# Kernel optimization log

Measured on AMD Instinct MI355X. Metric: run time of the kernel, lower is better.

Reference implementation:

```python
import jax, jax.numpy as jnp
import numpy as np

B, T, C = 4, 2048, 1024
H, HS = 16, 64  # n_heads, head_size; H*HS == C


def setup_inputs() -> dict:
    key = jax.random.key(0)
    ks = jax.random.split(key, 6)
    s = 0.02
    x = jax.random.normal(ks[0], (B, T, C), dtype=jnp.float32)
    Wq = jax.random.normal(ks[1], (H, C, HS), dtype=jnp.float32) * s
    Wk = jax.random.normal(ks[2], (H, C, HS), dtype=jnp.float32) * s
    Wv = jax.random.normal(ks[3], (H, C, HS), dtype=jnp.float32) * s
    Wo = jax.random.normal(ks[4], (C, C), dtype=jnp.float32) * s
    bo = jnp.zeros((C,), dtype=jnp.float32)
    return {"x": x, "Wq": Wq, "Wk": Wk, "Wv": Wv, "Wo": Wo, "bo": bo}


def reference(x, Wq, Wk, Wv, Wo, bo):
    # batched multi-head causal attention (math identical to per-head loop)
    q = jnp.einsum('btc,hcd->bhtd', x, Wq)  # [B,H,T,HS]
    k = jnp.einsum('btc,hcd->bhtd', x, Wk)
    v = jnp.einsum('btc,hcd->bhtd', x, Wv)
    scale = 1.0 / jnp.sqrt(jnp.asarray(HS, x.dtype))
    scores = jnp.einsum('bhtd,bhsd->bhts', q, k) * scale  # [B,H,T,T]
    causal = jnp.tril(jnp.ones((T, T), dtype=bool))
    scores = jnp.where(causal, scores, jnp.asarray(-jnp.inf, scores.dtype))
    attn = jax.nn.softmax(scores, axis=-1)
    out = jnp.einsum('bhts,bhsd->bhtd', attn, v)  # [B,H,T,HS]
    # concat heads along feature dim (head order == module list order)
    out = out.transpose(0, 2, 1, 3).reshape(B, T, C)
    return out @ Wo.T + bo
```

## Files before the change

### kernel.cpp

```cpp
#include <hip/hip_runtime.h>

typedef __attribute__((ext_vector_type(8))) short v8s;
typedef __attribute__((ext_vector_type(4))) short v4s;
typedef __attribute__((ext_vector_type(4))) float v4f;

static __device__ __forceinline__ short f2bf(float f) {
  union { float f; unsigned u; } c; c.f = f;
  unsigned r = c.u + 0x7fffu + ((c.u >> 16) & 1u);
  return (short)(r >> 16);
}

static __device__ __forceinline__ unsigned pk_bf16(float a, float b) {
  union { float f; unsigned u; } ca, cb; ca.f = a; cb.f = b;
  return ((ca.u + 0x8000u) >> 16) | ((cb.u + 0x8000u) & 0xffff0000u);
}

#if __has_builtin(__builtin_amdgcn_exp2f)
#define EXP2(x) __builtin_amdgcn_exp2f(x)
#else
#define EXP2(x) exp2f(x)
#endif

#define GLDS(gp, lp) __builtin_amdgcn_global_load_lds( \
    (const __attribute__((address_space(1))) void*)(gp), \
    (__attribute__((address_space(3))) void*)(lp), 16, 0, 0)


__global__ __launch_bounds__(256) void cast_f32_bf16(const float* __restrict__ src,
                                                     short* __restrict__ dst) {
  int idx = (blockIdx.x * 256 + threadIdx.x) * 4;
  float4 v = *(const float4*)(src + idx);
  v4s o; o.x = f2bf(v.x); o.y = f2bf(v.y); o.z = f2bf(v.z); o.w = f2bf(v.w);
  *(v4s*)(dst + idx) = o;
}

__global__ __launch_bounds__(256) void build_wt(const float* __restrict__ Wq,
                                                const float* __restrict__ Wk,
                                                const float* __restrict__ Wv,
                                                short* __restrict__ Wt) {
  __shared__ float tile[64][65];
  int blk = blockIdx.x;
  int sel = blk >> 8, rest = blk & 255;
  int h = rest >> 4, kt = rest & 15;
  const float* W = (sel == 0) ? Wq : ((sel == 1) ? Wk : Wv);
  int k0 = kt * 64;
  int tid = threadIdx.x;
  for (int i = 0; i < 4; ++i) {
    int c = i * 256 + tid;
    int row = c >> 4, c4 = (c & 15) * 4;
    float4 v = *(const float4*)(W + (size_t)h * 65536 + (size_t)(k0 + row) * 64 + c4);
    tile[row][c4 + 0] = v.x; tile[row][c4 + 1] = v.y;
    tile[row][c4 + 2] = v.z; tile[row][c4 + 3] = v.w;
  }
  __syncthreads();
  for (int i = 0; i < 2; ++i) {
    int c = i * 256 + tid;
    int d = c >> 3, k8 = (c & 7) * 8;
    v8s o;
    for (int j = 0; j < 8; ++j) o[j] = f2bf(tile[k8 + j][d]);
    *(v8s*)(Wt + (size_t)(sel * 1024 + h * 64 + d) * 1024 + k0 + k8) = o;
  }
}

__global__ __launch_bounds__(256) void transpose_v(const short* __restrict__ V,
                                                   short* __restrict__ Vt) {
  __shared__ short tile[64][72];
  int bh = blockIdx.x >> 5, tt = blockIdx.x & 31;
  int t0 = tt * 64;
  int tid = threadIdx.x;
  for (int i = 0; i < 2; ++i) {
    int c = i * 256 + tid;
    int row = c >> 3, col8 = (c & 7) * 8;
    v8s v = *(const v8s*)(V + ((size_t)(bh * 2048 + t0 + row)) * 64 + col8);
    *(v8s*)&tile[row][col8] = v;
  }
  __syncthreads();
  for (int i = 0; i < 2; ++i) {
    int c = i * 256 + tid;
    int d = c >> 3, t8 = (c & 7) * 8;
    v8s o;
    for (int j = 0; j < 8; ++j) o[j] = tile[t8 + j][d];
    *(v8s*)(Vt + ((size_t)(bh * 64 + d)) * 2048 + t0 + t8) = o;
  }
}


__global__ __launch_bounds__(256) void gemm_qkv(const short* __restrict__ Xb,
                                                const short* __restrict__ Wt,
                                                short* __restrict__ Qo,
                                                short* __restrict__ Ko,
                                                short* __restrict__ Vo) {
  __shared__ short lA[128 * 32];
  __shared__ short lB[128 * 32];
  const int tid = threadIdx.x;
  const int lane = tid & 63, quad = lane >> 4, l16 = lane & 15;
  const int wave = tid >> 6;
  const int m0 = blockIdx.x * 128, n0 = blockIdx.y * 128;
  const int wm = (wave >> 1) * 64, wn = (wave & 1) * 64;
  v4f acc[4][4];
  for (int i = 0; i < 4; ++i)
    for (int j = 0; j < 4; ++j) acc[i][j] = (v4f){0.f, 0.f, 0.f, 0.f};

  for (int k0 = 0; k0 < 1024; k0 += 32) {
    __syncthreads();
    for (int i = 0; i < 2; ++i) {
      int c = i * 256 + tid;
      int row = c >> 2, kc = c & 3;
      GLDS(Xb + (size_t)(m0 + row) * 1024 + k0 + kc * 8, lA + c * 8);
      GLDS(Wt + (size_t)(n0 + row) * 1024 + k0 + kc * 8, lB + c * 8);
    }
    __syncthreads();
    v8s a[4], b[4];
    for (int mt = 0; mt < 4; ++mt) a[mt] = *(const v8s*)&lA[(wm + mt * 16 + l16) * 32 + quad * 8];
    for (int nt = 0; nt < 4; ++nt) b[nt] = *(const v8s*)&lB[(wn + nt * 16 + l16) * 32 + quad * 8];
    for (int mt = 0; mt < 4; ++mt)
      for (int nt = 0; nt < 4; ++nt)
        acc[mt][nt] = __builtin_amdgcn_mfma_f32_16x16x32_bf16(a[mt], b[nt], acc[mt][nt], 0, 0, 0);
  }

  int selu = n0 >> 10;
  short* obase = (selu == 0) ? Qo : ((selu == 1) ? Ko : Vo);
  for (int nt = 0; nt < 4; ++nt) {
    int n = n0 + wn + nt * 16 + l16;
    int hd = n & 1023;
    int h = hd >> 6, d = hd & 63;
    for (int mt = 0; mt < 4; ++mt)
      for (int r = 0; r < 4; ++r) {
        int m = m0 + wm + mt * 16 + quad * 4 + r;
        int b_ = m >> 11, t = m & 2047;
        obase[(size_t)((b_ * 16 + h) * 2048 + t) * 64 + d] = f2bf(acc[mt][nt][r]);
      }
  }
}


__global__ __launch_bounds__(256, 2) void attn(const short* __restrict__ Q,
                                               const short* __restrict__ K,
                                               const short* __restrict__ Vt,
                                               short* __restrict__ AO) {
  __shared__ short lK[64 * 64];
  __shared__ short lV[64 * 64];
  __shared__ short lP[4 * 32 * 72];
  const int tid = threadIdx.x;
  const int w = tid >> 6, lane = tid & 63, quad = lane >> 4, l16 = lane & 15;
  const int bh = blockIdx.x & 63, pr = blockIdx.x >> 6;
  const float kexp = 0.18033688011112042f;
  const unsigned psel = 0x07060302u;
  short* pw = lP + w * (32 * 72);
  const size_t qkbase = (size_t)bh * 2048 * 64;
  const size_t vtbase = (size_t)bh * 64 * 2048;
  const int b_ = bh >> 4, h = bh & 15;

  const int r0 = tid >> 3, cp = tid & 7;
  const int cl0 = cp ^ (r0 & 7);
  const int r1 = r0 + 32;
  const int cl1 = cp ^ (r1 & 7);

  const int swz = l16 & 7;
  const int ph0 = (quad ^ swz) * 8;
  const int ph1 = ((quad + 4) ^ swz) * 8;

  for (int phase = 0; phase < 2; ++phase) {
    const int c = phase ? (15 - pr) : pr;
    const int qc = c * 128 + w * 32;

    v8s bQ[2][2];
#pragma unroll
    for (int qs = 0; qs < 2; ++qs) {
      const short* qb = Q + qkbase + (size_t)(qc + qs * 16 + l16) * 64 + quad * 8;
      bQ[qs][0] = *(const v8s*)(qb);
      bQ[qs][1] = *(const v8s*)(qb + 32);
    }
    v4f accO[2][4];
#pragma unroll
    for (int qs = 0; qs < 2; ++qs)
      for (int g = 0; g < 4; ++g) accO[qs][g] = (v4f){0.f, 0.f, 0.f, 0.f};
    float lrun[2] = {0.f, 0.f};

    const int nst = 2 * c + 2;
    for (int kt = 0; kt < nst; ++kt) {
      const int kb = kt * 64;
      __syncthreads();
      GLDS(K + qkbase + (size_t)(kb + r0) * 64 + cl0 * 8, lK + tid * 8);
      GLDS(K + qkbase + (size_t)(kb + r1) * 64 + cl1 * 8, lK + tid * 8 + 2048);
      GLDS(Vt + vtbase + (size_t)r0 * 2048 + kb + cl0 * 8, lV + tid * 8);
      GLDS(Vt + vtbase + (size_t)r1 * 2048 + kb + cl1 * 8, lV + tid * 8 + 2048);
      __syncthreads();

      const bool act0 = kb < qc + 16;
      const bool act1 = kb < qc + 32;
      if (!act1) continue;

      v8s aK[4][2];
#pragma unroll
      for (int mt = 0; mt < 4; ++mt) {
        const short* kr = lK + (mt * 16 + l16) * 64;
        aK[mt][0] = *(const v8s*)(kr + ph0);
        aK[mt][1] = *(const v8s*)(kr + ph1);
      }
#pragma unroll
      for (int qs = 0; qs < 2; ++qs) {
        if (qs == 0 ? !act0 : false) continue;
        const int rbase = qc + qs * 16;
        v4f sT[4];
#pragma unroll
        for (int mt = 0; mt < 4; ++mt) {
          v4f t = (v4f){0.f, 0.f, 0.f, 0.f};
          t = __builtin_amdgcn_mfma_f32_16x16x32_bf16(aK[mt][0], bQ[qs][0], t, 0, 0, 0);
          t = __builtin_amdgcn_mfma_f32_16x16x32_bf16(aK[mt][1], bQ[qs][1], t, 0, 0, 0);
          sT[mt] = t;
        }
        if (kb + 63 >= rbase) {
          const int kq = kb + quad * 4 - (rbase + l16);
#pragma unroll
          for (int mt = 0; mt < 4; ++mt)
#pragma unroll
            for (int r = 0; r < 4; ++r)
              if (kq + mt * 16 + r > 0) sT[mt][r] = -__builtin_inff();
        }
        float ls = lrun[qs];
#pragma unroll
        for (int mt = 0; mt < 4; ++mt) {
          float p0 = EXP2(sT[mt][0] * kexp);
          float p1 = EXP2(sT[mt][1] * kexp);
          float p2 = EXP2(sT[mt][2] * kexp);
          float p3 = EXP2(sT[mt][3] * kexp);
          ls += (p0 + p1) + (p2 + p3);
          int2 dw;
          dw.x = (int)__builtin_amdgcn_perm(__float_as_uint(p1), __float_as_uint(p0), psel);
          dw.y = (int)__builtin_amdgcn_perm(__float_as_uint(p3), __float_as_uint(p2), psel);
          *(int2*)&pw[(qs * 16 + l16) * 72 + mt * 16 + quad * 4] = dw;
        }
        lrun[qs] = ls;
      }
      v8s aV[4][2];
#pragma unroll
      for (int g = 0; g < 4; ++g) {
        const short* vr = lV + (g * 16 + l16) * 64;
        aV[g][0] = *(const v8s*)(vr + ph0);
        aV[g][1] = *(const v8s*)(vr + ph1);
      }
#pragma unroll
      for (int qs = 0; qs < 2; ++qs) {
        if (qs == 0 ? !act0 : false) continue;
        v8s bP0 = *(const v8s*)&pw[(qs * 16 + l16) * 72 + quad * 8];
        v8s bP1 = *(const v8s*)&pw[(qs * 16 + l16) * 72 + 32 + quad * 8];
#pragma unroll
        for (int g = 0; g < 4; ++g) {
          accO[qs][g] = __builtin_amdgcn_mfma_f32_16x16x32_bf16(aV[g][0], bP0, accO[qs][g], 0, 0, 0);
          accO[qs][g] = __builtin_amdgcn_mfma_f32_16x16x32_bf16(aV[g][1], bP1, accO[qs][g], 0, 0, 0);
        }
      }
    }

#pragma unroll
    for (int qs = 0; qs < 2; ++qs) {
      float ls = lrun[qs];
      ls += __shfl_xor(ls, 16);
      ls += __shfl_xor(ls, 32);
      float inv = __builtin_amdgcn_rcpf(ls);
      int t = qc + qs * 16 + l16;
      short* ao = AO + ((size_t)(b_ * 2048 + t)) * 1024 + h * 64 + quad * 4;
#pragma unroll
      for (int g = 0; g < 4; ++g) {
        int2 dw;
        dw.x = (int)pk_bf16(accO[qs][g][0] * inv, accO[qs][g][1] * inv);
        dw.y = (int)pk_bf16(accO[qs][g][2] * inv, accO[qs][g][3] * inv);
        *(int2*)(ao + g * 16) = dw;
      }
    }
  }
}


__global__ __launch_bounds__(256) void gemm_out(const short* __restrict__ AO,
                                                const short* __restrict__ Wot,
                                                const float* __restrict__ bo,
                                                float* __restrict__ out) {
  __shared__ short lA[128 * 32];
  __shared__ short lB[128 * 32];
  const int tid = threadIdx.x;
  const int lane = tid & 63, quad = lane >> 4, l16 = lane & 15;
  const int wave = tid >> 6;
  const int m0 = blockIdx.x * 128, n0 = blockIdx.y * 128;
  const int wm = (wave >> 1) * 64, wn = (wave & 1) * 64;
  v4f acc[4][4];
  for (int i = 0; i < 4; ++i)
    for (int j = 0; j < 4; ++j) acc[i][j] = (v4f){0.f, 0.f, 0.f, 0.f};

  for (int k0 = 0; k0 < 1024; k0 += 32) {
    __syncthreads();
    for (int i = 0; i < 2; ++i) {
      int c = i * 256 + tid;
      int row = c >> 2, kc = c & 3;
      GLDS(AO + (size_t)(m0 + row) * 1024 + k0 + kc * 8, lA + c * 8);
      GLDS(Wot + (size_t)(n0 + row) * 1024 + k0 + kc * 8, lB + c * 8);
    }
    __syncthreads();
    v8s a[4], b[4];
    for (int mt = 0; mt < 4; ++mt) a[mt] = *(const v8s*)&lA[(wm + mt * 16 + l16) * 32 + quad * 8];
    for (int nt = 0; nt < 4; ++nt) b[nt] = *(const v8s*)&lB[(wn + nt * 16 + l16) * 32 + quad * 8];
    for (int mt = 0; mt < 4; ++mt)
      for (int nt = 0; nt < 4; ++nt)
        acc[mt][nt] = __builtin_amdgcn_mfma_f32_16x16x32_bf16(a[mt], b[nt], acc[mt][nt], 0, 0, 0);
  }

  for (int nt = 0; nt < 4; ++nt) {
    int n = n0 + wn + nt * 16 + l16;
    float bias = bo[n];
    for (int mt = 0; mt < 4; ++mt)
      for (int r = 0; r < 4; ++r) {
        int m = m0 + wm + mt * 16 + quad * 4 + r;
        out[(size_t)m * 1024 + n] = acc[mt][nt][r] + bias;
      }
  }
}


extern "C" void kernel_launch(void* const* d_in, const int* in_sizes, int n_in,
                              void* d_out, int out_size, void* d_ws, size_t ws_size,
                              hipStream_t stream) {
  const float* x  = (const float*)d_in[0];
  const float* Wq = (const float*)d_in[1];
  const float* Wk = (const float*)d_in[2];
  const float* Wv = (const float*)d_in[3];
  const float* Wo = (const float*)d_in[4];
  const float* bo = (const float*)d_in[5];
  float* out = (float*)d_out;
  char* ws = (char*)d_ws;

  short* Xb  = (short*)(ws);
  short* Wt  = (short*)(ws + (16u << 20));
  short* Wot = (short*)(ws + (22u << 20));
  short* Q   = (short*)(ws + (24u << 20));
  short* K   = (short*)(ws + (40u << 20));
  short* V   = (short*)(ws + (56u << 20));
  short* Vt  = (short*)(ws + (72u << 20));

  cast_f32_bf16<<<8192, 256, 0, stream>>>(x, Xb);
  cast_f32_bf16<<<1024, 256, 0, stream>>>(Wo, Wot);
  build_wt<<<768, 256, 0, stream>>>(Wq, Wk, Wv, Wt);
  gemm_qkv<<<dim3(64, 24), 256, 0, stream>>>(Xb, Wt, Q, K, V);
  transpose_v<<<2048, 256, 0, stream>>>(V, Vt);
  attn<<<dim3(512), 256, 0, stream>>>(Q, K, Vt, Xb);
  gemm_out<<<dim3(64, 8), 256, 0, stream>>>(Xb, Wot, bo, out);
}
```

Baseline: 247.9 us.

## Fuse prep kernels and write V transposed directly from QKV GEMM

Merges the three cast and weight-transpose kernels into one launch with block-index dispatch. For V output tiles, the QKV GEMM swaps the MFMA operands so the accumulator comes out transposed and is stored straight into the Vt layout, which removes the separate transpose_v kernel and its extra write and read of V. This cuts launch count and memory traffic. The V-tile stores become per-lane writes along t, which may coalesce differently.

```diff
diff --git a/kernel.cpp b/kernel.cpp
--- a/kernel.cpp
+++ b/kernel.cpp
@@ -26,25 +26,32 @@
     (__attribute__((address_space(3))) void*)(lp), 16, 0, 0)
 
 
-__global__ __launch_bounds__(256) void cast_f32_bf16(const float* __restrict__ src,
-                                                     short* __restrict__ dst) {
-  int idx = (blockIdx.x * 256 + threadIdx.x) * 4;
-  float4 v = *(const float4*)(src + idx);
-  v4s o; o.x = f2bf(v.x); o.y = f2bf(v.y); o.z = f2bf(v.z); o.w = f2bf(v.w);
-  *(v4s*)(dst + idx) = o;
-}
-
-__global__ __launch_bounds__(256) void build_wt(const float* __restrict__ Wq,
-                                                const float* __restrict__ Wk,
-                                                const float* __restrict__ Wv,
-                                                short* __restrict__ Wt) {
+__global__ __launch_bounds__(256) void prep(const float* __restrict__ x,
+                                            const float* __restrict__ Wq,
+                                            const float* __restrict__ Wk,
+                                            const float* __restrict__ Wv,
+                                            const float* __restrict__ Wo,
+                                            short* __restrict__ Xb,
+                                            short* __restrict__ Wot,
+                                            short* __restrict__ Wt) {
   __shared__ float tile[64][65];
   int blk = blockIdx.x;
-  int sel = blk >> 8, rest = blk & 255;
+  int tid = threadIdx.x;
+  if (blk < 9216) {
+    const float* src = (blk < 8192) ? x : Wo;
+    short* dst = (blk < 8192) ? Xb : Wot;
+    int bb = (blk < 8192) ? blk : (blk - 8192);
+    int idx = (bb * 256 + tid) * 4;
+    float4 v = *(const float4*)(src + idx);
+    v4s o; o.x = f2bf(v.x); o.y = f2bf(v.y); o.z = f2bf(v.z); o.w = f2bf(v.w);
+    *(v4s*)(dst + idx) = o;
+    return;
+  }
+  int wblk = blk - 9216;
+  int sel = wblk >> 8, rest = wblk & 255;
   int h = rest >> 4, kt = rest & 15;
   const float* W = (sel == 0) ? Wq : ((sel == 1) ? Wk : Wv);
   int k0 = kt * 64;
-  int tid = threadIdx.x;
   for (int i = 0; i < 4; ++i) {
     int c = i * 256 + tid;
     int row = c >> 4, c4 = (c & 15) * 4;
@@ -62,34 +69,12 @@
   }
 }
 
-__global__ __launch_bounds__(256) void transpose_v(const short* __restrict__ V,
-                                                   short* __restrict__ Vt) {
-  __shared__ short tile[64][72];
-  int bh = blockIdx.x >> 5, tt = blockIdx.x & 31;
-  int t0 = tt * 64;
-  int tid = threadIdx.x;
-  for (int i = 0; i < 2; ++i) {
-    int c = i * 256 + tid;
-    int row = c >> 3, col8 = (c & 7) * 8;
-    v8s v = *(const v8s*)(V + ((size_t)(bh * 2048 + t0 + row)) * 64 + col8);
-    *(v8s*)&tile[row][col8] = v;
-  }
-  __syncthreads();
-  for (int i = 0; i < 2; ++i) {
-    int c = i * 256 + tid;
-    int d = c >> 3, t8 = (c & 7) * 8;
-    v8s o;
-    for (int j = 0; j < 8; ++j) o[j] = tile[t8 + j][d];
-    *(v8s*)(Vt + ((size_t)(bh * 64 + d)) * 2048 + t0 + t8) = o;
-  }
-}
-
 
 __global__ __launch_bounds__(256) void gemm_qkv(const short* __restrict__ Xb,
                                                 const short* __restrict__ Wt,
                                                 short* __restrict__ Qo,
                                                 short* __restrict__ Ko,
-                                                short* __restrict__ Vo) {
+                                                short* __restrict__ Vt) {
   __shared__ short lA[128 * 32];
   __shared__ short lB[128 * 32];
   const int tid = threadIdx.x;
@@ -97,6 +82,7 @@
   const int wave = tid >> 6;
   const int m0 = blockIdx.x * 128, n0 = blockIdx.y * 128;
   const int wm = (wave >> 1) * 64, wn = (wave & 1) * 64;
+  const bool vblk = (n0 >= 2048);
   v4f acc[4][4];
   for (int i = 0; i < 4; ++i)
     for (int j = 0; j < 4; ++j) acc[i][j] = (v4f){0.f, 0.f, 0.f, 0.f};
@@ -113,22 +99,41 @@
     v8s a[4], b[4];
     for (int mt = 0; mt < 4; ++mt) a[mt] = *(const v8s*)&lA[(wm + mt * 16 + l16) * 32 + quad * 8];
     for (int nt = 0; nt < 4; ++nt) b[nt] = *(const v8s*)&lB[(wn + nt * 16 + l16) * 32 + quad * 8];
-    for (int mt = 0; mt < 4; ++mt)
-      for (int nt = 0; nt < 4; ++nt)
-        acc[mt][nt] = __builtin_amdgcn_mfma_f32_16x16x32_bf16(a[mt], b[nt], acc[mt][nt], 0, 0, 0);
-  }
-
-  int selu = n0 >> 10;
-  short* obase = (selu == 0) ? Qo : ((selu == 1) ? Ko : Vo);
-  for (int nt = 0; nt < 4; ++nt) {
-    int n = n0 + wn + nt * 16 + l16;
-    int hd = n & 1023;
-    int h = hd >> 6, d = hd & 63;
-    for (int mt = 0; mt < 4; ++mt)
+    if (!vblk) {
+      for (int mt = 0; mt < 4; ++mt)
+        for (int nt = 0; nt < 4; ++nt)
+          acc[mt][nt] = __builtin_amdgcn_mfma_f32_16x16x32_bf16(a[mt], b[nt], acc[mt][nt], 0, 0, 0);
+    } else {
+      for (int mt = 0; mt < 4; ++mt)
+        for (int nt = 0; nt < 4; ++nt)
+          acc[mt][nt] = __builtin_amdgcn_mfma_f32_16x16x32_bf16(b[nt], a[mt], acc[mt][nt], 0, 0, 0);
+    }
+  }
+
+  if (!vblk) {
+    short* obase = (n0 < 1024) ? Qo : Ko;
+    for (int nt = 0; nt < 4; ++nt) {
+      int n = n0 + wn + nt * 16 + l16;
+      int hd = n & 1023;
+      int h = hd >> 6, d = hd & 63;
+      for (int mt = 0; mt < 4; ++mt)
+        for (int r = 0; r < 4; ++r) {
+          int m = m0 + wm + mt * 16 + quad * 4 + r;
+          int b_ = m >> 11, t = m & 2047;
+          obase[(size_t)((b_ * 16 + h) * 2048 + t) * 64 + d] = f2bf(acc[mt][nt][r]);
+        }
+    }
+  } else {
+    for (int nt = 0; nt < 4; ++nt)
       for (int r = 0; r < 4; ++r) {
-        int m = m0 + wm + mt * 16 + quad * 4 + r;
-        int b_ = m >> 11, t = m & 2047;
-        obase[(size_t)((b_ * 16 + h) * 2048 + t) * 64 + d] = f2bf(acc[mt][nt][r]);
+        int n = n0 + wn + nt * 16 + quad * 4 + r;
+        int hd = n & 1023;
+        int h = hd >> 6, d = hd & 63;
+        for (int mt = 0; mt < 4; ++mt) {
+          int m = m0 + wm + mt * 16 + l16;
+          int b_ = m >> 11, t = m & 2047;
+          Vt[(size_t)((b_ * 16 + h) * 64 + d) * 2048 + t] = f2bf(acc[mt][nt][r]);
+        }
       }
   }
 }
@@ -334,14 +339,10 @@
   short* Wot = (short*)(ws + (22u << 20));
   short* Q   = (short*)(ws + (24u << 20));
   short* K   = (short*)(ws + (40u << 20));
-  short* V   = (short*)(ws + (56u << 20));
-  short* Vt  = (short*)(ws + (72u << 20));
-
-  cast_f32_bf16<<<8192, 256, 0, stream>>>(x, Xb);
-  cast_f32_bf16<<<1024, 256, 0, stream>>>(Wo, Wot);
-  build_wt<<<768, 256, 0, stream>>>(Wq, Wk, Wv, Wt);
-  gemm_qkv<<<dim3(64, 24), 256, 0, stream>>>(Xb, Wt, Q, K, V);
-  transpose_v<<<2048, 256, 0, stream>>>(V, Vt);
+  short* Vt  = (short*)(ws + (56u << 20));
+
+  prep<<<9984, 256, 0, stream>>>(x, Wq, Wk, Wv, Wo, Xb, Wot, Wt);
+  gemm_qkv<<<dim3(64, 24), 256, 0, stream>>>(Xb, Wt, Q, K, Vt);
   attn<<<dim3(512), 256, 0, stream>>>(Q, K, Vt, Xb);
   gemm_out<<<dim3(64, 8), 256, 0, stream>>>(Xb, Wot, bo, out);
 }
```

Result: slower. 296.5 us (+19.6%).
